# Kernel optimization log

Measured on AMD Instinct MI355X. Metric: run time of the kernel, lower is better.

Reference implementation:

```python
import jax, jax.numpy as jnp
import numpy as np

B = 8192       # Monte Carlo paths
NSTEP = 30     # Euler time steps
D = 100        # z_dim / number of assets
H1 = 110
H2 = 110
T = NSTEP - 1  # number of subnets
DT = np.float32(1.0 / NSTEP)
R = np.float32(0.05)   # riskfree
EPS = np.float32(1e-3) # Keras BatchNormalization epsilon


def setup_inputs() -> dict:
    key = jax.random.key(0)
    ks = jax.random.split(key, 25)
    f = jnp.float32
    X = jax.random.normal(ks[0], (B, NSTEP, D), f)
    DWs = jax.random.normal(ks[1], (B, NSTEP, D), f) * jnp.sqrt(DT)
    sigmas = jax.random.uniform(ks[2], (D,), f, 0.1, 0.4)
    y_init = jax.random.uniform(ks[3], (1,), f, 0.0, 1.0)
    z_init = jax.random.uniform(ks[4], (1, D), f, -0.1, 0.1)
    W1 = jax.random.normal(ks[5], (T, D, H1), f) / np.sqrt(D).astype(np.float32)
    W2 = jax.random.normal(ks[6], (T, H1, H2), f) / np.sqrt(H1).astype(np.float32)
    W3 = jax.random.normal(ks[7], (T, H2, D), f) / np.sqrt(H2).astype(np.float32)
    dims = [D, H1, H2, D]
    bn = {}
    for j, dim in enumerate(dims):
        bn[f"g{j}"] = 1.0 + 0.1 * jax.random.normal(ks[8 + 4 * j], (T, dim), f)
        bn[f"b{j}"] = 0.05 * jax.random.normal(ks[9 + 4 * j], (T, dim), f)
        bn[f"m{j}"] = 0.1 * jax.random.normal(ks[10 + 4 * j], (T, dim), f)
        bn[f"v{j}"] = jax.random.uniform(ks[11 + 4 * j], (T, dim), f, 0.5, 1.5)
    return dict(X=X, DWs=DWs, sigmas=sigmas, y_init=y_init, z_init=z_init,
                W1=W1, W2=W2, W3=W3, **bn)


def _bn(x, g, b, m, v):
    # Keras BatchNormalization, inference mode
    return (x - m) * jax.lax.rsqrt(v + EPS) * g + b


def _subnet(x, p):
    (w1, w2, w3, g0, b0, m0, v0, g1, b1, m1, v1,
     g2, b2, m2, v2, g3, b3, m3, v3) = p
    x = _bn(x, g0, b0, m0, v0)
    x = jax.nn.relu(x @ w1)
    x = _bn(x, g1, b1, m1, v1)
    x = jax.nn.relu(x @ w2)
    x = _bn(x, g2, b2, m2, v2)
    x = x @ w3
    return _bn(x, g3, b3, m3, v3)


def reference(X, DWs, sigmas, y_init, z_init, W1, W2, W3,
              g0, b0, m0, v0, g1, b1, m1, v1,
              g2, b2, m2, v2, g3, b3, m3, v3):
    nb = X.shape[0]
    Y0 = jnp.ones((nb, 1), X.dtype) * y_init            # [B,1]
    Z0 = jnp.ones((nb, 1), X.dtype) * z_init            # [B,D]

    def step(carry, xs):
        Y, Z = carry
        Xi, Xn, DWi, p = xs
        Y = Y + R * Y * DT + jnp.sum(sigmas * Xi * Z * DWi, axis=1, keepdims=True)
        Z = _subnet(Xn, p)
        return (Y, Z), None

    params = (W1, W2, W3, g0, b0, m0, v0, g1, b1, m1, v1,
              g2, b2, m2, v2, g3, b3, m3, v3)  # each leading dim T
    xs = (jnp.moveaxis(X[:, :T], 1, 0),        # [T,B,D]
          jnp.moveaxis(X[:, 1:T + 1], 1, 0),   # [T,B,D]
          jnp.moveaxis(DWs[:, :T], 1, 0),      # [T,B,D]
          params)
    (Y, Z), _ = jax.lax.scan(step, (Y0, Z0), xs)
    # final step: X[:,-2,:] with DWs[:,-1,:]
    Y = Y + R * Y * DT + jnp.sum(sigmas * X[:, -2, :] * Z * DWs[:, -1, :],
                                 axis=1, keepdims=True)
    return Y
```

## Files before the change

kernel.cpp:

```cpp
#include <hip/hip_runtime.h>

typedef unsigned short ushort_t;
typedef __attribute__((ext_vector_type(8))) short s16x8;
typedef __attribute__((ext_vector_type(4))) float f32x4;

#define B_PATHS 8192
#define NSTEP   30
#define DD      100
#define HH      110
#define TT      29
#define ROWSTR  3000
#define LDK     136
#define WFRAGSZ 14336
#define DT_C    (1.0f/30.0f)
#define R_C     0.05f
#define EPS_C   1e-3f

__device__ __forceinline__ ushort_t f2bf(float f) {
  unsigned u = __float_as_uint(f);
  u = u + 0x7FFFu + ((u >> 16) & 1u);
  return (ushort_t)(u >> 16);
}
__device__ __forceinline__ float bf2f(ushort_t u) {
  return __uint_as_float(((unsigned)u) << 16);
}

__global__ void prep_kernel(const float* __restrict__ W1, const float* __restrict__ W2,
                            const float* __restrict__ W3,
                            const float* g0, const float* b0, const float* m0, const float* v0,
                            const float* g1, const float* b1, const float* m1, const float* v1,
                            const float* g2, const float* b2, const float* m2, const float* v2,
                            const float* g3, const float* b3, const float* m3, const float* v3,
                            ushort_t* __restrict__ wprep, float* __restrict__ bprep)
{
  const int mat = blockIdx.x, t = blockIdx.y, tid = threadIdx.x;
  __shared__ __align__(16) float wsh[110*110];
  __shared__ float sin_[112], hin_[112], sout_[112], hout_[112];

  int Kr, Nr; const float* W; const float *g, *bb, *mm, *vv;
  if (mat == 0)      { Kr = 100; Nr = 110; W = W1 + t*11000; g = g0+t*100; bb = b0+t*100; mm = m0+t*100; vv = v0+t*100; }
  else if (mat == 1) { Kr = 110; Nr = 110; W = W2 + t*12100; g = g1+t*110; bb = b1+t*110; mm = m1+t*110; vv = v1+t*110; }
  else               { Kr = 110; Nr = 100; W = W3 + t*11000; g = g2+t*110; bb = b2+t*110; mm = m2+t*110; vv = v2+t*110; }

  if (tid < Kr) {
    float s = g[tid] * rsqrtf(vv[tid] + EPS_C);
    sin_[tid] = s; hin_[tid] = bb[tid] - mm[tid]*s;
  }
  if (mat == 2 && tid < Nr) {
    float s = g3[t*100+tid] * rsqrtf(v3[t*100+tid] + EPS_C);
    sout_[tid] = s; hout_[tid] = b3[t*100+tid] - m3[t*100+tid]*s;
  }
  {
    const int n4 = (Kr*Nr) >> 2;
    for (int i = tid; i < n4; i += 256)
      ((float4*)wsh)[i] = ((const float4*)W)[i];
  }
  __syncthreads();

  if (tid < 128) {
    float c = 0.f;
    if (tid < Nr) {
      for (int k = 0; k < Kr; ++k) c += hin_[k] * wsh[k*Nr + tid];
      if (mat == 2) c = c * sout_[tid] + hout_[tid];
    }
    bprep[(t*3 + mat)*128 + tid] = c;
  }

  ushort_t* wo = wprep + (size_t)(t*3 + mat) * WFRAGSZ;
  for (int ch = tid; ch < 1792; ch += 256) {
    const int lane = ch & 63, ntkb = ch >> 6;
    const int nt = ntkb % 7, kb = ntkb / 7;
    const int n  = nt*16 + (lane & 15);
    const int k0 = kb*32 + (lane >> 4)*8;
    ushort_t tmp[8];
#pragma unroll
    for (int j = 0; j < 8; ++j) {
      const int k = k0 + j;
      float v = 0.f;
      if (n < Nr && k < Kr) {
        v = sin_[k] * wsh[k*Nr + n];
        if (mat == 2) v *= sout_[n];
      }
      tmp[j] = f2bf(v);
    }
    ushort4 lo; lo.x = tmp[0]; lo.y = tmp[1]; lo.z = tmp[2]; lo.w = tmp[3];
    ushort4 hi; hi.x = tmp[4]; hi.y = tmp[5]; hi.z = tmp[6]; hi.w = tmp[7];
    *(ushort4*)(wo + ch*8)     = lo;
    *(ushort4*)(wo + ch*8 + 4) = hi;
  }
}

__device__ __forceinline__ void mlp_stage16(ushort_t* act, const ushort_t* __restrict__ wfrag,
                                            const float* __restrict__ biasg,
                                            int wrow, int lane, int lrow, int quad, bool relu)
{
  f32x4 acc[7];
  const f32x4 z4 = {0.f, 0.f, 0.f, 0.f};
#pragma unroll
  for (int nt = 0; nt < 7; ++nt) acc[nt] = z4;

  s16x8 a[4];
#pragma unroll
  for (int kb = 0; kb < 4; ++kb)
    a[kb] = *(const s16x8*)(act + (wrow + lrow)*LDK + kb*32 + quad*8);

#pragma unroll
  for (int kb = 0; kb < 4; ++kb) {
    s16x8 b[7];
#pragma unroll
    for (int nt = 0; nt < 7; ++nt)
      b[nt] = *(const s16x8*)(wfrag + ((kb*7 + nt)*64 + lane)*8);
#pragma unroll
    for (int nt = 0; nt < 7; ++nt)
      acc[nt] = __builtin_amdgcn_mfma_f32_16x16x32_bf16(a[kb], b[nt], acc[nt], 0, 0, 0);
  }

#pragma unroll
  for (int nt = 0; nt < 7; ++nt) {
    const int col = nt*16 + lrow;
    const float bv = biasg[col];
#pragma unroll
    for (int r = 0; r < 4; ++r) {
      float u = acc[nt][r] + bv;
      if (relu) u = u > 0.f ? u : 0.f;
      act[(wrow + quad*4 + r)*LDK + col] = f2bf(u);
    }
  }
#pragma unroll
  for (int r = 0; r < 4; ++r)
    act[(wrow + quad*4 + r)*LDK + 112 + lrow] = 0;
}

__global__ __launch_bounds__(128, 8)
void subnet_kernel(const float* __restrict__ X, const float* __restrict__ DW,
                   const float* __restrict__ sigmas,
                   const ushort_t* __restrict__ wprep, const float* __restrict__ bprep,
                   float* __restrict__ sbuf)
{
  __shared__ __align__(16) ushort_t act[32*LDK];

  const int tid  = threadIdx.x;
  const int t    = blockIdx.y;
  const int m0   = blockIdx.x * 32;
  const int lane = tid & 63;
  const int wrow = (tid >> 6) * 16;
  const int lrow = lane & 15, quad = lane >> 4;

  {
    const int c  = lane & 31;
    const int r0 = lane >> 5;
#pragma unroll
    for (int i = 0; i < 8; ++i) {
      const int r = r0 + i*2;
      ushort4 u; u.x = 0; u.y = 0; u.z = 0; u.w = 0;
      if (c < 25) {
        const float4 v = *(const float4*)(X + (size_t)(m0 + wrow + r)*ROWSTR + (t+1)*DD + c*4);
        u.x = f2bf(v.x); u.y = f2bf(v.y); u.z = f2bf(v.z); u.w = f2bf(v.w);
      }
      *(ushort4*)(act + (wrow + r)*LDK + c*4) = u;
    }
  }

  const ushort_t* wf = wprep + (size_t)(t*3) * WFRAGSZ;
  const float*    bg = bprep + (t*3) * 128;

  mlp_stage16(act, wf,             bg,       wrow, lane, lrow, quad, true);
  mlp_stage16(act, wf + WFRAGSZ,   bg + 128, wrow, lane, lrow, quad, true);
  mlp_stage16(act, wf + 2*WFRAGSZ, bg + 256, wrow, lane, lrow, quad, false);

  {
    const int row  = wrow + (lane >> 2);
    const int part = lane & 3;
    const int b    = m0 + row;
    const int xt   = (t == TT - 1) ? (NSTEP - 2) : (t + 1);
    const float* xr = X  + (size_t)b*ROWSTR + xt*DD;
    const float* dr = DW + (size_t)b*ROWSTR + (t+1)*DD;
    float p = 0.f;
#pragma unroll
    for (int g = part; g < 25; g += 4) {
      const float4 xv = *(const float4*)(xr + g*4);
      const float4 dv = *(const float4*)(dr + g*4);
      const float4 sg = *(const float4*)(sigmas + g*4);
      const ushort4 zu = *(const ushort4*)(act + row*LDK + g*4);
      p += sg.x*xv.x*dv.x*bf2f(zu.x);
      p += sg.y*xv.y*dv.y*bf2f(zu.y);
      p += sg.z*xv.z*dv.z*bf2f(zu.z);
      p += sg.w*xv.w*dv.w*bf2f(zu.w);
    }
    p += __shfl_xor(p, 1, 64);
    p += __shfl_xor(p, 2, 64);
    if (part == 0)
      sbuf[(size_t)(t+1)*B_PATHS + b] = p;
  }
}

__global__ __launch_bounds__(256)
void y_kernel(const float* __restrict__ X, const float* __restrict__ DW,
              const float* __restrict__ sigmas, const float* __restrict__ y_init,
              const float* __restrict__ z_init, const float* __restrict__ sbuf,
              float* __restrict__ out)
{
  const int tid  = threadIdx.x;
  const int row  = tid >> 3, part = tid & 7;
  const int b    = blockIdx.x * 32 + row;
  const float* xr = X + (size_t)b * ROWSTR;
  const float* dr = DW + (size_t)b * ROWSTR;
  float p = 0.f;
#pragma unroll
  for (int g = part; g < 25; g += 8) {
    const float4 xv = *(const float4*)(xr + g*4);
    const float4 dv = *(const float4*)(dr + g*4);
    const float4 sg = *(const float4*)(sigmas + g*4);
    const float4 zv = *(const float4*)(z_init + g*4);
    p += sg.x*xv.x*zv.x*dv.x;
    p += sg.y*xv.y*zv.y*dv.y;
    p += sg.z*xv.z*zv.z*dv.z;
    p += sg.w*xv.w*zv.w*dv.w;
  }
  p += __shfl_xor(p, 1, 64);
  p += __shfl_xor(p, 2, 64);
  p += __shfl_xor(p, 4, 64);

  const float G = 1.f + R_C*DT_C;
  float ss = 0.f;
#pragma unroll
  for (int tau = 1 + part; tau < NSTEP; tau += 8)
    ss += sbuf[(size_t)tau*B_PATHS + b] * __powf(G, (float)(NSTEP - 1 - tau));
  ss += __shfl_xor(ss, 1, 64);
  ss += __shfl_xor(ss, 2, 64);
  ss += __shfl_xor(ss, 4, 64);

  if (part == 0)
    out[b] = y_init[0]*__powf(G, 30.f) + p*__powf(G, 29.f) + ss;
}

extern "C" void kernel_launch(void* const* d_in, const int* in_sizes, int n_in,
                              void* d_out, int out_size, void* d_ws, size_t ws_size,
                              hipStream_t stream) {
  const float* X      = (const float*)d_in[0];
  const float* DWs    = (const float*)d_in[1];
  const float* sigmas = (const float*)d_in[2];
  const float* y_init = (const float*)d_in[3];
  const float* z_init = (const float*)d_in[4];
  const float* W1     = (const float*)d_in[5];
  const float* W2     = (const float*)d_in[6];
  const float* W3     = (const float*)d_in[7];
  const float* bn[16];
  for (int i = 0; i < 16; ++i) bn[i] = (const float*)d_in[8 + i];

  char* ws = (char*)d_ws;
  ushort_t* wprep = (ushort_t*)ws;
  float*    bprep = (float*)(ws + 2494464);
  float*    sbuf  = (float*)(ws + 2539008);
  float*    out   = (float*)d_out;

  prep_kernel<<<dim3(3, TT), 256, 0, stream>>>(
      W1, W2, W3,
      bn[0], bn[1], bn[2], bn[3],  bn[4], bn[5], bn[6], bn[7],
      bn[8], bn[9], bn[10], bn[11], bn[12], bn[13], bn[14], bn[15],
      wprep, bprep);
  subnet_kernel<<<dim3(B_PATHS/32, TT), 128, 0, stream>>>(
      X, DWs, sigmas, wprep, bprep, sbuf);
  y_kernel<<<dim3(B_PATHS/32), 256, 0, stream>>>(
      X, DWs, sigmas, y_init, z_init, sbuf, out);
}
```

Measured before the change: 344.3 us.

## Stage subnet weight fragments in LDS with register prefetch, 64-row blocks

Blocks are widened from 32 rows and 2 waves to 64 rows and 4 waves. Each layer's weight fragments are now loaded cooperatively into shared memory, and the next layer's weights are prefetched into registers while the current layer's MFMAs run. Previously every wave read its B fragments straight from global or L2. This cuts redundant global weight traffic and overlaps the loads with compute, but adds barriers, about 28KB more LDS per block and extra register pressure under launch bounds of 3 blocks.

```diff
diff --git a/kernel.cpp b/kernel.cpp
--- a/kernel.cpp
+++ b/kernel.cpp
@@ -90,7 +90,7 @@
   }
 }
 
-__device__ __forceinline__ void mlp_stage16(ushort_t* act, const ushort_t* __restrict__ wfrag,
+__device__ __forceinline__ void mlp_stage16(ushort_t* act, const ushort_t* wbuf,
                                             const float* __restrict__ biasg,
                                             int wrow, int lane, int lrow, int quad, bool relu)
 {
@@ -109,7 +109,7 @@
     s16x8 b[7];
 #pragma unroll
     for (int nt = 0; nt < 7; ++nt)
-      b[nt] = *(const s16x8*)(wfrag + ((kb*7 + nt)*64 + lane)*8);
+      b[nt] = *(const s16x8*)(wbuf + ((kb*7 + nt)*64 + lane)*8);
 #pragma unroll
     for (int nt = 0; nt < 7; ++nt)
       acc[nt] = __builtin_amdgcn_mfma_f32_16x16x32_bf16(a[kb], b[nt], acc[nt], 0, 0, 0);
@@ -131,42 +131,66 @@
     act[(wrow + quad*4 + r)*LDK + 112 + lrow] = 0;
 }
 
-__global__ __launch_bounds__(128, 8)
+__global__ __launch_bounds__(256, 3)
 void subnet_kernel(const float* __restrict__ X, const float* __restrict__ DW,
                    const float* __restrict__ sigmas,
                    const ushort_t* __restrict__ wprep, const float* __restrict__ bprep,
                    float* __restrict__ sbuf)
 {
-  __shared__ __align__(16) ushort_t act[32*LDK];
+  __shared__ __align__(16) ushort_t act[64*LDK];
+  __shared__ __align__(16) ushort_t wbuf[WFRAGSZ];
 
   const int tid  = threadIdx.x;
   const int t    = blockIdx.y;
-  const int m0   = blockIdx.x * 32;
+  const int m0   = blockIdx.x * 64;
   const int lane = tid & 63;
   const int wrow = (tid >> 6) * 16;
   const int lrow = lane & 15, quad = lane >> 4;
 
-  {
-    const int c  = lane & 31;
-    const int r0 = lane >> 5;
-#pragma unroll
-    for (int i = 0; i < 8; ++i) {
-      const int r = r0 + i*2;
-      ushort4 u; u.x = 0; u.y = 0; u.z = 0; u.w = 0;
-      if (c < 25) {
-        const float4 v = *(const float4*)(X + (size_t)(m0 + wrow + r)*ROWSTR + (t+1)*DD + c*4);
-        u.x = f2bf(v.x); u.y = f2bf(v.y); u.z = f2bf(v.z); u.w = f2bf(v.w);
-      }
-      *(ushort4*)(act + (wrow + r)*LDK + c*4) = u;
-    }
-  }
-
   const ushort_t* wf = wprep + (size_t)(t*3) * WFRAGSZ;
   const float*    bg = bprep + (t*3) * 128;
 
-  mlp_stage16(act, wf,             bg,       wrow, lane, lrow, quad, true);
-  mlp_stage16(act, wf + WFRAGSZ,   bg + 128, wrow, lane, lrow, quad, true);
-  mlp_stage16(act, wf + 2*WFRAGSZ, bg + 256, wrow, lane, lrow, quad, false);
+  s16x8 wst[7];
+#pragma unroll
+  for (int j = 0; j < 7; ++j)
+    wst[j] = *(const s16x8*)(wf + (j*256 + tid)*8);
+
+  for (int jj = tid; jj < 64*32; jj += 256) {
+    const int r = jj >> 5, c = jj & 31;
+    ushort4 u; u.x = 0; u.y = 0; u.z = 0; u.w = 0;
+    if (c < 25) {
+      const float4 v = *(const float4*)(X + (size_t)(m0 + r)*ROWSTR + (t+1)*DD + c*4);
+      u.x = f2bf(v.x); u.y = f2bf(v.y); u.z = f2bf(v.z); u.w = f2bf(v.w);
+    }
+    *(ushort4*)(act + r*LDK + c*4) = u;
+  }
+
+#pragma unroll
+  for (int j = 0; j < 7; ++j)
+    *(s16x8*)(wbuf + (j*256 + tid)*8) = wst[j];
+  __syncthreads();
+
+#pragma unroll
+  for (int j = 0; j < 7; ++j)
+    wst[j] = *(const s16x8*)(wf + WFRAGSZ + (j*256 + tid)*8);
+  mlp_stage16(act, wbuf, bg, wrow, lane, lrow, quad, true);
+  __syncthreads();
+#pragma unroll
+  for (int j = 0; j < 7; ++j)
+    *(s16x8*)(wbuf + (j*256 + tid)*8) = wst[j];
+  __syncthreads();
+
+#pragma unroll
+  for (int j = 0; j < 7; ++j)
+    wst[j] = *(const s16x8*)(wf + 2*WFRAGSZ + (j*256 + tid)*8);
+  mlp_stage16(act, wbuf, bg + 128, wrow, lane, lrow, quad, true);
+  __syncthreads();
+#pragma unroll
+  for (int j = 0; j < 7; ++j)
+    *(s16x8*)(wbuf + (j*256 + tid)*8) = wst[j];
+  __syncthreads();
+
+  mlp_stage16(act, wbuf, bg + 256, wrow, lane, lrow, quad, false);
 
   {
     const int row  = wrow + (lane >> 2);
@@ -259,7 +283,7 @@
       bn[0], bn[1], bn[2], bn[3],  bn[4], bn[5], bn[6], bn[7],
       bn[8], bn[9], bn[10], bn[11], bn[12], bn[13], bn[14], bn[15],
       wprep, bprep);
-  subnet_kernel<<<dim3(B_PATHS/32, TT), 128, 0, stream>>>(
+  subnet_kernel<<<dim3(B_PATHS/64, TT), 256, 0, stream>>>(
       X, DWs, sigmas, wprep, bprep, sbuf);
   y_kernel<<<dim3(B_PATHS/32), 256, 0, stream>>>(
       X, DWs, sigmas, y_init, z_init, sbuf, out);
```

After: 322.2 us. 6.4% less time.
